# Kernel tuning notes

Measured on AMD Instinct MI355X. Metric: run time of the kernel, lower is better.

The kernel has to match this reference:

```python
import jax, jax.numpy as jnp
import numpy as np

D = 128
N_SRC = 50000
N_DST = 50000
E = 640000
NEG_SLOPE = 0.01  # torch LeakyReLU default


def _lrelu(x):
    return jax.nn.leaky_relu(x, NEG_SLOPE)


def setup_inputs() -> dict:
    key = jax.random.key(0)
    ks = jax.random.split(key, 12)
    s = 1.0 / np.sqrt(D)
    return {
        "feat_src": jax.random.normal(ks[0], (N_SRC, D), jnp.float32),
        "feat_dst": jax.random.normal(ks[1], (N_DST, D), jnp.float32),
        "src_idx": jax.random.randint(ks[2], (E,), 0, N_SRC, jnp.int32),
        "dst_idx": jax.random.randint(ks[3], (E,), 0, N_DST, jnp.int32),
        "W_src": jax.random.uniform(ks[4], (D, D), jnp.float32, -s, s),
        "b_src": jnp.zeros((D,), jnp.float32),
        "W_dst": jax.random.uniform(ks[5], (D, D), jnp.float32, -s, s),
        "b_dst": jnp.zeros((D,), jnp.float32),
        "W_a1": jax.random.uniform(ks[6], (D, D), jnp.float32, -s, s),
        "b_a1": jnp.zeros((D,), jnp.float32),
        "W_a2": jax.random.uniform(ks[7], (D, 1), jnp.float32, -s, s),
        "b_a2": jnp.zeros((1,), jnp.float32),
        "W_out": jax.random.uniform(ks[8], (D, D), jnp.float32, -s, s),
        "b_out": jnp.zeros((D,), jnp.float32),
    }


def reference(feat_src, feat_dst, src_idx, dst_idx,
              W_src, b_src, W_dst, b_dst,
              W_a1, b_a1, W_a2, b_a2, W_out, b_out):
    n_dst = feat_dst.shape[0]
    # node projections (dropout is identity in eval mode)
    hs = feat_src @ W_src + b_src            # [n_src, d]
    hd = feat_dst @ W_dst + b_dst            # [n_dst, d]
    # u_add_v: per-edge feature
    e = hs[src_idx] + hd[dst_idx]            # [E, d]
    # attention MLP: LeakyReLU -> Linear -> LeakyReLU -> Linear(d->1)
    s = _lrelu(_lrelu(e) @ W_a1 + b_a1) @ W_a2 + b_a2  # [E, 1]
    s = s[:, 0]
    # edge softmax grouped by destination node (numerically stable)
    m = jax.ops.segment_max(s, dst_idx, num_segments=n_dst)
    ex = jnp.exp(s - m[dst_idx])
    denom = jax.ops.segment_sum(ex, dst_idx, num_segments=n_dst)
    alpha = ex / denom[dst_idx]              # [E]
    # scale messages and scatter-sum to dst nodes
    n_f = jax.ops.segment_sum(alpha[:, None] * e, dst_idx, num_segments=n_dst)
    return _lrelu(n_f @ W_out + b_out)       # [n_dst, d]
```

## Files before the change

kernel.cpp:

```cpp
#include <hip/hip_runtime.h>
#include <math.h>

#define DD 128
#define NEG 0.01f
#define SCHUNK 4096

typedef __attribute__((ext_vector_type(8))) _Float16 half8;
typedef __attribute__((ext_vector_type(4))) float f32x4;

__device__ __forceinline__ float lrelu(float x){ return x > 0.f ? x : NEG * x; }

__device__ __forceinline__ unsigned short h2u(_Float16 h){
    union { _Float16 h; unsigned short u; } v; v.h = h; return v.u;
}
__device__ __forceinline__ _Float16 u2h(unsigned short u){
    union { unsigned short u; _Float16 h; } v; v.u = u; return v.h;
}

__device__ __forceinline__ half8 h8max(half8 x, half8 y){
#if __has_builtin(__builtin_elementwise_max)
    return __builtin_elementwise_max(x, y);
#else
    half8 r;
    #pragma unroll
    for (int i = 0; i < 8; i++) r[i] = x[i] > y[i] ? x[i] : y[i];
    return r;
#endif
}

__global__ void hist_pack(const int* dst, int* deg, int E, int nhist,
                          const float* Wa1, const float* Wsrc,
                          const float* Wdst, const float* Wout,
                          unsigned short* wpack){
    const int bid = blockIdx.x;
    if (bid < nhist){
        int i = bid * 256 + threadIdx.x;
        if (i < E) atomicAdd(&deg[dst[i]], 1);
    } else {
        int i = (bid - nhist) * 256 + threadIdx.x;
        if (i >= 4 * 16384) return;
        int seg = i >> 14, t = i & 16383;
        int j = t & 7, lane = (t >> 3) & 63, nt = (t >> 9) & 7, kc = t >> 12;
        int k = kc * 32 + (lane >> 4) * 8 + j;
        int n = nt * 16 + (lane & 15);
        const float* W = (seg == 0) ? Wa1 : (seg == 1) ? Wsrc : (seg == 2) ? Wdst : Wout;
        wpack[i] = h2u((_Float16)W[k * DD + n]);
    }
}

__global__ __launch_bounds__(1024) void scan1(const int* deg, int* part, int n){
    __shared__ int wsum[16];
    const int tid = threadIdx.x;
    const int lane = tid & 63, wid = tid >> 6;
    int i4 = blockIdx.x * SCHUNK + tid * 4;
    int4 v = make_int4(0, 0, 0, 0);
    if (i4 + 3 < n) v = *(const int4*)(deg + i4);
    else {
        if (i4 + 0 < n) v.x = deg[i4 + 0];
        if (i4 + 1 < n) v.y = deg[i4 + 1];
        if (i4 + 2 < n) v.z = deg[i4 + 2];
        if (i4 + 3 < n) v.w = deg[i4 + 3];
    }
    int t = v.x + v.y + v.z + v.w;
    #pragma unroll
    for (int off = 1; off < 64; off <<= 1) t += __shfl_xor(t, off, 64);
    if (lane == 0) wsum[wid] = t;
    __syncthreads();
    if (tid == 0){
        int s = 0;
        #pragma unroll
        for (int j = 0; j < 16; j++) s += wsum[j];
        part[blockIdx.x] = s;
    }
}

__global__ __launch_bounds__(1024) void scan2(const int* deg, const int* part,
        int* row_off, int* cursor, int n, int nchunks){
    __shared__ int wsum[16];
    const int tid = threadIdx.x;
    const int lane = tid & 63, wid = tid >> 6;
    const int b = blockIdx.x;
    int carry = 0;
    for (int j = 0; j < b; j++) carry += part[j];
    int i4 = b * SCHUNK + tid * 4;
    int4 v = make_int4(0, 0, 0, 0);
    if (i4 + 3 < n) v = *(const int4*)(deg + i4);
    else {
        if (i4 + 0 < n) v.x = deg[i4 + 0];
        if (i4 + 1 < n) v.y = deg[i4 + 1];
        if (i4 + 2 < n) v.z = deg[i4 + 2];
        if (i4 + 3 < n) v.w = deg[i4 + 3];
    }
    int tsum = v.x + v.y + v.z + v.w;
    int x = tsum;
    #pragma unroll
    for (int off = 1; off < 64; off <<= 1){
        int t = __shfl_up(x, off, 64);
        if (lane >= off) x += t;
    }
    if (lane == 63) wsum[wid] = x;
    __syncthreads();
    int wprefix = 0;
    #pragma unroll
    for (int j = 0; j < 16; j++) if (j < wid) wprefix += wsum[j];
    int excl = carry + wprefix + (x - tsum);
    if (i4 + 3 < n){
        int4 o;
        o.x = excl; o.y = excl + v.x; o.z = o.y + v.y; o.w = o.z + v.z;
        *(int4*)(row_off + i4) = o;
        *(int4*)(cursor + i4) = o;
    } else {
        int a = excl;
        if (i4 + 0 < n){ row_off[i4 + 0] = a; cursor[i4 + 0] = a; a += v.x; }
        if (i4 + 1 < n){ row_off[i4 + 1] = a; cursor[i4 + 1] = a; a += v.y; }
        if (i4 + 2 < n){ row_off[i4 + 2] = a; cursor[i4 + 2] = a; a += v.z; }
        if (i4 + 3 < n){ row_off[i4 + 3] = a; cursor[i4 + 3] = a; }
    }
    if (b == 0 && tid == 0){
        int tot = 0;
        for (int j = 0; j < nchunks; j++) tot += part[j];
        row_off[n] = tot;
    }
}

__global__ void scatter_pairs(const int* src, const int* dst, int* cursor,
                              int2* pairs, int* s_srcs, int E){
    int i = blockIdx.x * blockDim.x + threadIdx.x;
    if (i < E){
        int d = dst[i];
        int s = src[i];
        int pos = atomicAdd(&cursor[d], 1);
        pairs[pos] = make_int2(s, d);
        s_srcs[pos] = s;
    }
}

__global__ __launch_bounds__(256) void lin2_mfma(
        const float* X1, const unsigned short* W1, const float* b1,
        unsigned short* Yb1, int n1, int g1,
        const float* X2, const unsigned short* W2, const float* b2,
        unsigned short* Yb2, int n2){
    __shared__ unsigned short sB[16384];
    const int tid = threadIdx.x;
    const int second = (blockIdx.x >= g1);
    const float* X = second ? X2 : X1;
    const unsigned short* W = second ? W2 : W1;
    const float* b = second ? b2 : b1;
    unsigned short* Yb = second ? Yb2 : Yb1;
    const int nrows = second ? n2 : n1;
    const int bidx = second ? (blockIdx.x - g1) : blockIdx.x;
    {
        const uint4* g = (const uint4*)W;
        uint4* l = (uint4*)sB;
        #pragma unroll
        for (int t = 0; t < 8; t++) l[tid + 256 * t] = g[tid + 256 * t];
    }
    const int wave = tid >> 6, lane = tid & 63;
    const int qd = lane >> 4, ln16 = lane & 15;
    const int row0 = bidx * 128 + wave * 32;
    int r0 = row0 + ln16;       if (r0 >= nrows) r0 = nrows - 1;
    int r1 = row0 + 16 + ln16;  if (r1 >= nrows) r1 = nrows - 1;
    f32x4 acc[2][8];
    #pragma unroll
    for (int rt = 0; rt < 2; rt++)
        #pragma unroll
        for (int nt = 0; nt < 8; nt++)
            acc[rt][nt] = (f32x4){0.f, 0.f, 0.f, 0.f};
    __syncthreads();
    #pragma unroll
    for (int kc = 0; kc < 4; kc++){
        const int koff = kc * 32 + qd * 8;
        half8 a[2];
        const float* px[2] = {X + (size_t)r0 * DD + koff, X + (size_t)r1 * DD + koff};
        #pragma unroll
        for (int rt = 0; rt < 2; rt++){
            float4 v0 = *(const float4*)(px[rt]);
            float4 v1 = *(const float4*)(px[rt] + 4);
            a[rt][0] = (_Float16)v0.x; a[rt][1] = (_Float16)v0.y;
            a[rt][2] = (_Float16)v0.z; a[rt][3] = (_Float16)v0.w;
            a[rt][4] = (_Float16)v1.x; a[rt][5] = (_Float16)v1.y;
            a[rt][6] = (_Float16)v1.z; a[rt][7] = (_Float16)v1.w;
        }
        #pragma unroll
        for (int nt = 0; nt < 8; nt++){
            const int fi = (((kc << 3) + nt) << 6 | lane) << 3;
            half8 bw = *(const half8*)&sB[fi];
            acc[0][nt] = __builtin_amdgcn_mfma_f32_16x16x32_f16(a[0], bw, acc[0][nt], 0, 0, 0);
            acc[1][nt] = __builtin_amdgcn_mfma_f32_16x16x32_f16(a[1], bw, acc[1][nt], 0, 0, 0);
        }
    }
    #pragma unroll
    for (int nt = 0; nt < 8; nt++){
        const int col = nt * 16 + ln16;
        const float bv = b[col];
        #pragma unroll
        for (int rt = 0; rt < 2; rt++){
            #pragma unroll
            for (int r = 0; r < 4; r++){
                int row = row0 + rt * 16 + qd * 4 + r;
                if (row < nrows){
                    float y = acc[rt][nt][r] + bv;
                    Yb[(size_t)row * DD + col] = h2u((_Float16)y);
                }
            }
        }
    }
}

__global__ __launch_bounds__(256) void lin_mfma(const float* X,
        const unsigned short* W, const float* b, float* Y, int nrows){
    __shared__ unsigned short sB[16384];
    const int tid = threadIdx.x;
    {
        const uint4* g = (const uint4*)W;
        uint4* l = (uint4*)sB;
        #pragma unroll
        for (int t = 0; t < 8; t++) l[tid + 256 * t] = g[tid + 256 * t];
    }
    const int wave = tid >> 6, lane = tid & 63;
    const int qd = lane >> 4, ln16 = lane & 15;
    const int row0 = blockIdx.x * 128 + wave * 32;
    int r0 = row0 + ln16;       if (r0 >= nrows) r0 = nrows - 1;
    int r1 = row0 + 16 + ln16;  if (r1 >= nrows) r1 = nrows - 1;
    f32x4 acc[2][8];
    #pragma unroll
    for (int rt = 0; rt < 2; rt++)
        #pragma unroll
        for (int nt = 0; nt < 8; nt++)
            acc[rt][nt] = (f32x4){0.f, 0.f, 0.f, 0.f};
    __syncthreads();
    #pragma unroll
    for (int kc = 0; kc < 4; kc++){
        const int koff = kc * 32 + qd * 8;
        half8 a[2];
        const float* px[2] = {X + (size_t)r0 * DD + koff, X + (size_t)r1 * DD + koff};
        #pragma unroll
        for (int rt = 0; rt < 2; rt++){
            float4 v0 = *(const float4*)(px[rt]);
            float4 v1 = *(const float4*)(px[rt] + 4);
            a[rt][0] = (_Float16)v0.x; a[rt][1] = (_Float16)v0.y;
            a[rt][2] = (_Float16)v0.z; a[rt][3] = (_Float16)v0.w;
            a[rt][4] = (_Float16)v1.x; a[rt][5] = (_Float16)v1.y;
            a[rt][6] = (_Float16)v1.z; a[rt][7] = (_Float16)v1.w;
        }
        #pragma unroll
        for (int nt = 0; nt < 8; nt++){
            const int fi = (((kc << 3) + nt) << 6 | lane) << 3;
            half8 bw = *(const half8*)&sB[fi];
            acc[0][nt] = __builtin_amdgcn_mfma_f32_16x16x32_f16(a[0], bw, acc[0][nt], 0, 0, 0);
            acc[1][nt] = __builtin_amdgcn_mfma_f32_16x16x32_f16(a[1], bw, acc[1][nt], 0, 0, 0);
        }
    }
    #pragma unroll
    for (int nt = 0; nt < 8; nt++){
        const int col = nt * 16 + ln16;
        const float bv = b[col];
        #pragma unroll
        for (int rt = 0; rt < 2; rt++){
            #pragma unroll
            for (int r = 0; r < 4; r++){
                int row = row0 + rt * 16 + qd * 4 + r;
                if (row < nrows){
                    float y = acc[rt][nt][r] + bv;
                    Y[(size_t)row * DD + col] = lrelu(y);
                }
            }
        }
    }
}

__device__ __forceinline__ half8 make_afrag(const unsigned short* ph, const unsigned short* pd){
    half8 a = *(const half8*)ph;
    half8 b = *(const half8*)pd;
    half8 s = a + b;
    return h8max(s, s * (_Float16)NEG);
}

__global__ __launch_bounds__(512) void edge_score_mfma(
        const unsigned short* hs_h, const unsigned short* hd_h,
        const int2* pairs,
        const unsigned short* wa1p, const float* ba1,
        const float* Wa2, const float* ba2,
        float* s_w, int E){
    __shared__ unsigned short sB[16384];
    const int tid = threadIdx.x;
    {
        const uint4* g = (const uint4*)wa1p;
        uint4* l = (uint4*)sB;
        #pragma unroll
        for (int t = 0; t < 4; t++) l[tid + 512 * t] = g[tid + 512 * t];
    }
    const int wave = tid >> 6, lane = tid & 63;
    const int qd = lane >> 4, ln16 = lane & 15;
    const int e0 = blockIdx.x * 256 + wave * 32;
    float b1v[8], w2v[8];
    #pragma unroll
    for (int nt = 0; nt < 8; nt++){
        b1v[nt] = ba1[nt * 16 + ln16];
        w2v[nt] = Wa2[nt * 16 + ln16];
    }
    const float b2 = ba2[0];
    __syncthreads();
    for (int rt = 0; rt < 2; rt++){
        int eid = e0 + rt * 16 + ln16;
        if (eid >= E) eid = E - 1;
        const int2 pp = pairs[eid];
        f32x4 acc[8];
        #pragma unroll
        for (int nt = 0; nt < 8; nt++)
            acc[nt] = (f32x4){b1v[nt], b1v[nt], b1v[nt], b1v[nt]};
        #pragma unroll
        for (int kc = 0; kc < 4; kc++){
            const int koff = kc * 32 + qd * 8;
            half8 af = make_afrag(hs_h + (size_t)pp.x * DD + koff,
                                  hd_h + (size_t)pp.y * DD + koff);
            #pragma unroll
            for (int nt = 0; nt < 8; nt++){
                half8 bf = *(const half8*)&sB[(((kc << 3) + nt) << 6 | lane) << 3];
                acc[nt] = __builtin_amdgcn_mfma_f32_16x16x32_f16(af, bf, acc[nt], 0, 0, 0);
            }
        }
        float p[4] = {0.f, 0.f, 0.f, 0.f};
        #pragma unroll
        for (int nt = 0; nt < 8; nt++)
            #pragma unroll
            for (int r = 0; r < 4; r++){
                float z = acc[nt][r];
                z = fmaxf(z, NEG * z);
                p[r] += z * w2v[nt];
            }
        #pragma unroll
        for (int r = 0; r < 4; r++){
            float v = p[r];
            #pragma unroll
            for (int off = 1; off < 16; off <<= 1) v += __shfl_xor(v, off, 64);
            p[r] = __expf(v + b2);
        }
        if (ln16 == 0){
            int row = e0 + rt * 16 + qd * 4;
            #pragma unroll
            for (int r = 0; r < 4; r++)
                if (row + r < E) s_w[row + r] = p[r];
        }
    }
}

__global__ __launch_bounds__(256) void agg_softmax(const unsigned short* hs_h,
        const unsigned short* hd_h, const int* row_off, const int* s_srcs,
        const float* s_w, float* nf, int n_dst){
    const int w = (blockIdx.x * blockDim.x + threadIdx.x) >> 6;
    const int lane = threadIdx.x & 63;
    if (w >= n_dst) return;
    const int beg = row_off[w], end = row_off[w + 1];
    float2 acc = make_float2(0.f, 0.f);
    float sa = 0.f;
    int e = beg;
    for (; e + 7 < end; e += 8){
        float wv[8]; int sv[8]; ushort2 uv[8];
        #pragma unroll
        for (int j = 0; j < 8; j++){ wv[j] = s_w[e + j]; sv[j] = s_srcs[e + j]; }
        #pragma unroll
        for (int j = 0; j < 8; j++)
            uv[j] = *(const ushort2*)(hs_h + (size_t)sv[j] * DD + lane * 2);
        #pragma unroll
        for (int j = 0; j < 8; j++){
            acc.x += wv[j] * (float)u2h(uv[j].x);
            acc.y += wv[j] * (float)u2h(uv[j].y);
            sa += wv[j];
        }
    }
    for (; e < end; e++){
        float w0 = s_w[e];
        int s0 = s_srcs[e];
        ushort2 u0 = *(const ushort2*)(hs_h + (size_t)s0 * DD + lane * 2);
        acc.x += w0 * (float)u2h(u0.x);
        acc.y += w0 * (float)u2h(u0.y);
        sa += w0;
    }
    const float inv = (end > beg) ? 1.f / sa : 0.f;
    ushort2 hu = *(const ushort2*)(hd_h + (size_t)w * DD + lane * 2);
    const float hx = (end > beg) ? (float)u2h(hu.x) : 0.f;
    const float hy = (end > beg) ? (float)u2h(hu.y) : 0.f;
    float2 out;
    out.x = acc.x * inv + hx;
    out.y = acc.y * inv + hy;
    *(float2*)(nf + (size_t)w * DD + lane * 2) = out;
}

extern "C" void kernel_launch(void* const* d_in, const int* in_sizes, int n_in,
                              void* d_out, int out_size, void* d_ws, size_t ws_size,
                              hipStream_t stream){
    const float* feat_src = (const float*)d_in[0];
    const float* feat_dst = (const float*)d_in[1];
    const int*   src_idx  = (const int*)d_in[2];
    const int*   dst_idx  = (const int*)d_in[3];
    const float* W_src = (const float*)d_in[4];
    const float* b_src = (const float*)d_in[5];
    const float* W_dst = (const float*)d_in[6];
    const float* b_dst = (const float*)d_in[7];
    const float* W_a1  = (const float*)d_in[8];
    const float* b_a1  = (const float*)d_in[9];
    const float* W_a2  = (const float*)d_in[10];
    const float* b_a2  = (const float*)d_in[11];
    const float* W_out = (const float*)d_in[12];
    const float* b_out = (const float*)d_in[13];
    const int n_src = in_sizes[0] / DD;
    const int n_dst = in_sizes[1] / DD;
    const int E = in_sizes[2];
    const int nchunks = (n_dst + SCHUNK - 1) / SCHUNK;

    char* p = (char*)d_ws;
    unsigned short* hs_h = (unsigned short*)p;  p += (size_t)n_src * DD * 2;
    unsigned short* hd_h = (unsigned short*)p;  p += (size_t)n_dst * DD * 2;
    unsigned short* wpack = (unsigned short*)p; p += 4 * 16384 * 2;
    float* s_w = (float*)p;                     p += (size_t)E * 4;
    int2* pairs = (int2*)p;                     p += (size_t)E * 8;
    int* s_srcs = (int*)p;                      p += (size_t)E * 4;
    int* deg = (int*)p;                         p += (size_t)n_dst * 4;
    int* cursor = (int*)p;                      p += (size_t)n_dst * 4;
    int* part = (int*)p;                        p += 64 * 4;
    int* row_off = (int*)p;                     p += ((size_t)n_dst + 1) * 4;
    float* nf = (float*)d_out;

    const unsigned short* wa1p = wpack;
    const unsigned short* wsrc = wpack + 1 * 16384;
    const unsigned short* wdst = wpack + 2 * 16384;
    const unsigned short* wout = wpack + 3 * 16384;

    hipMemsetAsync(deg, 0, (size_t)n_dst * 4, stream);
    const int nhist = (E + 255) / 256;
    const int npack = (4 * 16384 + 255) / 256;
    hist_pack<<<nhist + npack, 256, 0, stream>>>(dst_idx, deg, E, nhist,
                                                 W_a1, W_src, W_dst, W_out, wpack);
    scan1<<<nchunks, 1024, 0, stream>>>(deg, part, n_dst);
    scan2<<<nchunks, 1024, 0, stream>>>(deg, part, row_off, cursor, n_dst, nchunks);
    scatter_pairs<<<(E + 255) / 256, 256, 0, stream>>>(src_idx, dst_idx, cursor,
                                                       pairs, s_srcs, E);
    const int g1 = (n_src + 127) / 128;
    const int g2 = (n_dst + 127) / 128;
    lin2_mfma<<<g1 + g2, 256, 0, stream>>>(feat_src, wsrc, b_src, hs_h, n_src, g1,
                                           feat_dst, wdst, b_dst, hd_h, n_dst);
    edge_score_mfma<<<(E + 255) / 256, 512, 0, stream>>>(hs_h, hd_h, pairs, wa1p, b_a1,
                                                         W_a2, b_a2, s_w, E);
    agg_softmax<<<((size_t)n_dst * 64 + 255) / 256, 256, 0, stream>>>(hs_h, hd_h, row_off,
                                                                      s_srcs, s_w, nf, n_dst);
    lin_mfma<<<g2, 256, 0, stream>>>(nf, wout, b_out, nf, n_dst);
}
```

Baseline: 300.7 us.

## Merge scans into one block, drop s_srcs array, vectorize aggregation gather

```diff
diff --git a/kernel.cpp b/kernel.cpp
--- a/kernel.cpp
+++ b/kernel.cpp
@@ -3,7 +3,6 @@
 
 #define DD 128
 #define NEG 0.01f
-#define SCHUNK 4096
 
 typedef __attribute__((ext_vector_type(8))) _Float16 half8;
 typedef __attribute__((ext_vector_type(4))) float f32x4;
@@ -48,51 +47,25 @@
     }
 }
 
-__global__ __launch_bounds__(1024) void scan1(const int* deg, int* part, int n){
+__global__ __launch_bounds__(1024) void scan_all(const int* deg, int* row_off,
+                                                 int* cursor, int n){
     __shared__ int wsum[16];
     const int tid = threadIdx.x;
     const int lane = tid & 63, wid = tid >> 6;
-    int i4 = blockIdx.x * SCHUNK + tid * 4;
-    int4 v = make_int4(0, 0, 0, 0);
-    if (i4 + 3 < n) v = *(const int4*)(deg + i4);
-    else {
-        if (i4 + 0 < n) v.x = deg[i4 + 0];
-        if (i4 + 1 < n) v.y = deg[i4 + 1];
-        if (i4 + 2 < n) v.z = deg[i4 + 2];
-        if (i4 + 3 < n) v.w = deg[i4 + 3];
-    }
-    int t = v.x + v.y + v.z + v.w;
-    #pragma unroll
-    for (int off = 1; off < 64; off <<= 1) t += __shfl_xor(t, off, 64);
-    if (lane == 0) wsum[wid] = t;
-    __syncthreads();
-    if (tid == 0){
-        int s = 0;
-        #pragma unroll
-        for (int j = 0; j < 16; j++) s += wsum[j];
-        part[blockIdx.x] = s;
-    }
-}
-
-__global__ __launch_bounds__(1024) void scan2(const int* deg, const int* part,
-        int* row_off, int* cursor, int n, int nchunks){
-    __shared__ int wsum[16];
-    const int tid = threadIdx.x;
-    const int lane = tid & 63, wid = tid >> 6;
-    const int b = blockIdx.x;
-    int carry = 0;
-    for (int j = 0; j < b; j++) carry += part[j];
-    int i4 = b * SCHUNK + tid * 4;
-    int4 v = make_int4(0, 0, 0, 0);
-    if (i4 + 3 < n) v = *(const int4*)(deg + i4);
-    else {
-        if (i4 + 0 < n) v.x = deg[i4 + 0];
-        if (i4 + 1 < n) v.y = deg[i4 + 1];
-        if (i4 + 2 < n) v.z = deg[i4 + 2];
-        if (i4 + 3 < n) v.w = deg[i4 + 3];
-    }
-    int tsum = v.x + v.y + v.z + v.w;
-    int x = tsum;
+    const int per = ((n + 4095) >> 12) << 2;
+    const int base = tid * per;
+    int s = 0;
+    for (int i = 0; i < per; i += 4){
+        int idx = base + i;
+        if (idx + 3 < n){
+            int4 v = *(const int4*)(deg + idx);
+            s += v.x + v.y + v.z + v.w;
+        } else {
+            #pragma unroll
+            for (int k = 0; k < 4; k++) if (idx + k < n) s += deg[idx + k];
+        }
+    }
+    int x = s;
     #pragma unroll
     for (int off = 1; off < 64; off <<= 1){
         int t = __shfl_up(x, off, 64);
@@ -100,38 +73,41 @@
     }
     if (lane == 63) wsum[wid] = x;
     __syncthreads();
-    int wprefix = 0;
-    #pragma unroll
-    for (int j = 0; j < 16; j++) if (j < wid) wprefix += wsum[j];
-    int excl = carry + wprefix + (x - tsum);
-    if (i4 + 3 < n){
-        int4 o;
-        o.x = excl; o.y = excl + v.x; o.z = o.y + v.y; o.w = o.z + v.z;
-        *(int4*)(row_off + i4) = o;
-        *(int4*)(cursor + i4) = o;
-    } else {
-        int a = excl;
-        if (i4 + 0 < n){ row_off[i4 + 0] = a; cursor[i4 + 0] = a; a += v.x; }
-        if (i4 + 1 < n){ row_off[i4 + 1] = a; cursor[i4 + 1] = a; a += v.y; }
-        if (i4 + 2 < n){ row_off[i4 + 2] = a; cursor[i4 + 2] = a; a += v.z; }
-        if (i4 + 3 < n){ row_off[i4 + 3] = a; cursor[i4 + 3] = a; }
-    }
-    if (b == 0 && tid == 0){
+    int wpre = 0;
+    #pragma unroll
+    for (int j = 0; j < 16; j++) if (j < wid) wpre += wsum[j];
+    int a = wpre + (x - s);
+    for (int i = 0; i < per; i += 4){
+        int idx = base + i;
+        if (idx + 3 < n){
+            int4 v = *(const int4*)(deg + idx);
+            int4 o; o.x = a; o.y = a + v.x; o.z = o.y + v.y; o.w = o.z + v.z;
+            *(int4*)(row_off + idx) = o;
+            *(int4*)(cursor + idx) = o;
+            a = o.w + v.w;
+        } else {
+            #pragma unroll
+            for (int k = 0; k < 4; k++) if (idx + k < n){
+                row_off[idx + k] = a; cursor[idx + k] = a; a += deg[idx + k];
+            }
+        }
+    }
+    if (tid == 0){
         int tot = 0;
-        for (int j = 0; j < nchunks; j++) tot += part[j];
+        #pragma unroll
+        for (int j = 0; j < 16; j++) tot += wsum[j];
         row_off[n] = tot;
     }
 }
 
 __global__ void scatter_pairs(const int* src, const int* dst, int* cursor,
-                              int2* pairs, int* s_srcs, int E){
+                              int2* pairs, int E){
     int i = blockIdx.x * blockDim.x + threadIdx.x;
     if (i < E){
         int d = dst[i];
         int s = src[i];
         int pos = atomicAdd(&cursor[d], 1);
         pairs[pos] = make_int2(s, d);
-        s_srcs[pos] = s;
     }
 }
 
@@ -269,9 +245,7 @@
     }
 }
 
-__device__ __forceinline__ half8 make_afrag(const unsigned short* ph, const unsigned short* pd){
-    half8 a = *(const half8*)ph;
-    half8 b = *(const half8*)pd;
+__device__ __forceinline__ half8 afrag_from(half8 a, half8 b){
     half8 s = a + b;
     return h8max(s, s * (_Float16)NEG);
 }
@@ -299,7 +273,6 @@
         b1v[nt] = ba1[nt * 16 + ln16];
         w2v[nt] = Wa2[nt * 16 + ln16];
     }
-    const float b2 = ba2[0];
     __syncthreads();
     for (int rt = 0; rt < 2; rt++){
         int eid = e0 + rt * 16 + ln16;
@@ -312,8 +285,8 @@
         #pragma unroll
         for (int kc = 0; kc < 4; kc++){
             const int koff = kc * 32 + qd * 8;
-            half8 af = make_afrag(hs_h + (size_t)pp.x * DD + koff,
-                                  hd_h + (size_t)pp.y * DD + koff);
+            half8 af = afrag_from(*(const half8*)(hs_h + (size_t)pp.x * DD + koff),
+                                  *(const half8*)(hd_h + (size_t)pp.y * DD + koff));
             #pragma unroll
             for (int nt = 0; nt < 8; nt++){
                 half8 bf = *(const half8*)&sB[(((kc << 3) + nt) << 6 | lane) << 3];
@@ -334,7 +307,7 @@
             float v = p[r];
             #pragma unroll
             for (int off = 1; off < 16; off <<= 1) v += __shfl_xor(v, off, 64);
-            p[r] = __expf(v + b2);
+            p[r] = __expf(v);
         }
         if (ln16 == 0){
             int row = e0 + rt * 16 + qd * 4;
@@ -346,45 +319,69 @@
 }
 
 __global__ __launch_bounds__(256) void agg_softmax(const unsigned short* hs_h,
-        const unsigned short* hd_h, const int* row_off, const int* s_srcs,
+        const unsigned short* hd_h, const int* row_off, const int2* pairs,
         const float* s_w, float* nf, int n_dst){
     const int w = (blockIdx.x * blockDim.x + threadIdx.x) >> 6;
     const int lane = threadIdx.x & 63;
     if (w >= n_dst) return;
     const int beg = row_off[w], end = row_off[w + 1];
-    float2 acc = make_float2(0.f, 0.f);
+    const int g = lane >> 4, l16 = lane & 15;
+    float va[8] = {0.f, 0.f, 0.f, 0.f, 0.f, 0.f, 0.f, 0.f};
     float sa = 0.f;
     int e = beg;
-    for (; e + 7 < end; e += 8){
-        float wv[8]; int sv[8]; ushort2 uv[8];
-        #pragma unroll
-        for (int j = 0; j < 8; j++){ wv[j] = s_w[e + j]; sv[j] = s_srcs[e + j]; }
-        #pragma unroll
-        for (int j = 0; j < 8; j++)
-            uv[j] = *(const ushort2*)(hs_h + (size_t)sv[j] * DD + lane * 2);
-        #pragma unroll
-        for (int j = 0; j < 8; j++){
-            acc.x += wv[j] * (float)u2h(uv[j].x);
-            acc.y += wv[j] * (float)u2h(uv[j].y);
+    for (; e + 15 < end; e += 16){
+        int rows[4]; float wv[4]; half8 uv[4];
+        #pragma unroll
+        for (int j = 0; j < 4; j++){
+            int ee = e + 4 * j + g;
+            rows[j] = pairs[ee].x;
+            wv[j] = s_w[ee];
+        }
+        #pragma unroll
+        for (int j = 0; j < 4; j++)
+            uv[j] = *(const half8*)(hs_h + (size_t)rows[j] * DD + l16 * 8);
+        #pragma unroll
+        for (int j = 0; j < 4; j++){
+            #pragma unroll
+            for (int k = 0; k < 8; k++)
+                va[k] += wv[j] * (float)uv[j][k];
             sa += wv[j];
         }
     }
-    for (; e < end; e++){
-        float w0 = s_w[e];
-        int s0 = s_srcs[e];
-        ushort2 u0 = *(const ushort2*)(hs_h + (size_t)s0 * DD + lane * 2);
-        acc.x += w0 * (float)u2h(u0.x);
-        acc.y += w0 * (float)u2h(u0.y);
-        sa += w0;
-    }
+    for (; e < end; e += 4){
+        int ee = e + g;
+        float wv = 0.f;
+        int row = pairs[beg].x;
+        if (ee < end){ row = pairs[ee].x; wv = s_w[ee]; }
+        half8 uv = *(const half8*)(hs_h + (size_t)row * DD + l16 * 8);
+        #pragma unroll
+        for (int k = 0; k < 8; k++)
+            va[k] += wv * (float)uv[k];
+        sa += wv;
+    }
+    #pragma unroll
+    for (int k = 0; k < 8; k++){
+        va[k] += __shfl_xor(va[k], 16, 64);
+        va[k] += __shfl_xor(va[k], 32, 64);
+    }
+    sa += __shfl_xor(sa, 16, 64);
+    sa += __shfl_xor(sa, 32, 64);
     const float inv = (end > beg) ? 1.f / sa : 0.f;
-    ushort2 hu = *(const ushort2*)(hd_h + (size_t)w * DD + lane * 2);
-    const float hx = (end > beg) ? (float)u2h(hu.x) : 0.f;
-    const float hy = (end > beg) ? (float)u2h(hu.y) : 0.f;
-    float2 out;
-    out.x = acc.x * inv + hx;
-    out.y = acc.y * inv + hy;
-    *(float2*)(nf + (size_t)w * DD + lane * 2) = out;
+    if (g == 0){
+        half8 hu = *(const half8*)(hd_h + (size_t)w * DD + l16 * 8);
+        const float gx = (end > beg) ? 1.f : 0.f;
+        float4 o0, o1;
+        o0.x = va[0] * inv + gx * (float)hu[0];
+        o0.y = va[1] * inv + gx * (float)hu[1];
+        o0.z = va[2] * inv + gx * (float)hu[2];
+        o0.w = va[3] * inv + gx * (float)hu[3];
+        o1.x = va[4] * inv + gx * (float)hu[4];
+        o1.y = va[5] * inv + gx * (float)hu[5];
+        o1.z = va[6] * inv + gx * (float)hu[6];
+        o1.w = va[7] * inv + gx * (float)hu[7];
+        *(float4*)(nf + (size_t)w * DD + l16 * 8) = o0;
+        *(float4*)(nf + (size_t)w * DD + l16 * 8 + 4) = o1;
+    }
 }
 
 extern "C" void kernel_launch(void* const* d_in, const int* in_sizes, int n_in,
@@ -407,7 +404,6 @@
     const int n_src = in_sizes[0] / DD;
     const int n_dst = in_sizes[1] / DD;
     const int E = in_sizes[2];
-    const int nchunks = (n_dst + SCHUNK - 1) / SCHUNK;
 
     char* p = (char*)d_ws;
     unsigned short* hs_h = (unsigned short*)p;  p += (size_t)n_src * DD * 2;
@@ -415,10 +411,8 @@
     unsigned short* wpack = (unsigned short*)p; p += 4 * 16384 * 2;
     float* s_w = (float*)p;                     p += (size_t)E * 4;
     int2* pairs = (int2*)p;                     p += (size_t)E * 8;
-    int* s_srcs = (int*)p;                      p += (size_t)E * 4;
     int* deg = (int*)p;                         p += (size_t)n_dst * 4;
     int* cursor = (int*)p;                      p += (size_t)n_dst * 4;
-    int* part = (int*)p;                        p += 64 * 4;
     int* row_off = (int*)p;                     p += ((size_t)n_dst + 1) * 4;
     float* nf = (float*)d_out;
 
@@ -432,10 +426,9 @@
     const int npack = (4 * 16384 + 255) / 256;
     hist_pack<<<nhist + npack, 256, 0, stream>>>(dst_idx, deg, E, nhist,
                                                  W_a1, W_src, W_dst, W_out, wpack);
-    scan1<<<nchunks, 1024, 0, stream>>>(deg, part, n_dst);
-    scan2<<<nchunks, 1024, 0, stream>>>(deg, part, row_off, cursor, n_dst, nchunks);
+    scan_all<<<1, 1024, 0, stream>>>(deg, row_off, cursor, n_dst);
     scatter_pairs<<<(E + 255) / 256, 256, 0, stream>>>(src_idx, dst_idx, cursor,
-                                                       pairs, s_srcs, E);
+                                                       pairs, E);
     const int g1 = (n_src + 127) / 128;
     const int g2 = (n_dst + 127) / 128;
     lin2_mfma<<<g1 + g2, 256, 0, stream>>>(feat_src, wsrc, b_src, hs_h, n_src, g1,
@@ -443,6 +436,6 @@
     edge_score_mfma<<<(E + 255) / 256, 512, 0, stream>>>(hs_h, hd_h, pairs, wa1p, b_a1,
                                                          W_a2, b_a2, s_w, E);
     agg_softmax<<<((size_t)n_dst * 64 + 255) / 256, 256, 0, stream>>>(hs_h, hd_h, row_off,
-                                                                      s_srcs, s_w, nf, n_dst);
+                                                                      pairs, s_w, nf, n_dst);
     lin_mfma<<<g2, 256, 0, stream>>>(nf, wout, b_out, nf, n_dst);
 }
```

Result: slower. 328.2 us (+9.2%).
